# Optimization experiments

Hardware: AMD Instinct MI355X
Metric: run time of the kernel (lower is better)

## Reference

```python
import jax, jax.numpy as jnp
import numpy as np

DIM = 2048
N_HEADS = 32
N_KV_HEADS = 8
HEAD_DIM = 64
REPEATS = N_HEADS // N_KV_HEADS
SLIDING_WINDOW = 1024
EPS = 1e-6
B, T = 2, 2048


def _alibi_slopes(n):
    # n_heads=32 is a power of 2
    r = 2.0 ** (-8.0 / n)
    return jnp.asarray([r ** i for i in range(n)], dtype=jnp.float32)


def _rms_norm(x, w, eps):
    # RMSNorm over the last (flattened heads*head_dim) axis
    var = jnp.mean(x * x, axis=-1, keepdims=True)
    return x * jax.lax.rsqrt(var + eps) * w


def setup_inputs() -> dict:
    key = jax.random.key(0)
    ks = jax.random.split(key, 6)
    s = 0.02
    return {
        "x": jax.random.normal(ks[0], (B, T, DIM), jnp.float32),
        "wq": jax.random.normal(ks[1], (N_HEADS * HEAD_DIM, DIM), jnp.float32) * s,
        "wk": jax.random.normal(ks[2], (N_KV_HEADS * HEAD_DIM, DIM), jnp.float32) * s,
        "wv": jax.random.normal(ks[3], (N_KV_HEADS * HEAD_DIM, DIM), jnp.float32) * s,
        "wo": jax.random.normal(ks[4], (DIM, N_HEADS * HEAD_DIM), jnp.float32) * s,
        "q_norm_w": jnp.ones((N_HEADS * HEAD_DIM,), jnp.float32),
        "k_norm_w": jnp.ones((N_KV_HEADS * HEAD_DIM,), jnp.float32),
    }


def reference(x, wq, wk, wv, wo, q_norm_w, k_norm_w):
    bsz, seqlen, _ = x.shape
    xq = _rms_norm(x @ wq.T, q_norm_w, EPS)
    xk = _rms_norm(x @ wk.T, k_norm_w, EPS)
    xv = x @ wv.T
    xq = xq.reshape(bsz, seqlen, N_HEADS, HEAD_DIM).transpose(0, 2, 1, 3)  # b h t d
    xk = xk.reshape(bsz, seqlen, N_KV_HEADS, HEAD_DIM).transpose(0, 2, 1, 3)
    xv = xv.reshape(bsz, seqlen, N_KV_HEADS, HEAD_DIM).transpose(0, 2, 1, 3)
    # GQA: repeat_interleave kv heads
    xk = jnp.repeat(xk, REPEATS, axis=1)
    xv = jnp.repeat(xv, REPEATS, axis=1)

    pos = jnp.arange(seqlen)
    dist = pos[None, :] - pos[:, None]                     # [t,s] = s - t (<=0 on causal side)
    slopes = _alibi_slopes(N_HEADS)
    alibi = slopes[:, None, None] * dist.astype(jnp.float32)  # [h,t,s]
    allowed = (dist <= 0) & (dist >= -SLIDING_WINDOW)      # causal + sliding window
    bias = jnp.where(allowed[None], alibi, -jnp.inf)       # [h,t,s]

    scale = 1.0 / jnp.sqrt(jnp.asarray(HEAD_DIM, jnp.float32))
    scores = jnp.einsum("bhtd,bhsd->bhts", xq, xk) * scale + bias[None]
    attn = jax.nn.softmax(scores, axis=-1)
    out = jnp.einsum("bhts,bhsd->bhtd", attn, xv)          # [b,h,t,d]
    out = out.transpose(0, 2, 1, 3).reshape(bsz, seqlen, N_HEADS * HEAD_DIM)
    return out @ wo.T
```

## Files before the change

kernel.cpp:

```cpp
#include <hip/hip_runtime.h>


typedef _Float16 f16;
typedef __attribute__((ext_vector_type(8))) _Float16 f16x8;
typedef __attribute__((ext_vector_type(4))) _Float16 f16x4;
typedef __attribute__((ext_vector_type(4))) float f32x4;

#define T_ 2048
#define NH 32
#define NKV 8
#define HD 64
#define WINDOW 1024
#define EPS_ 1e-6f
#define LOG2E 1.44269504088896340736f
#define LDQKV 3072

__device__ inline void async16(void* lds, const void* g) {
  __builtin_amdgcn_global_load_lds(
      (const __attribute__((address_space(1))) unsigned int*)g,
      (__attribute__((address_space(3))) unsigned int*)lds, 16, 0, 0);
}

struct CvtArgs {
  const float* src[5];
  f16* dst[5];
  int n4[5];
};
__global__ __launch_bounds__(256) void cvt_multi(CvtArgs a) {
  const int seg = blockIdx.y;
  const float* in = a.src[seg];
  f16* out = a.dst[seg];
  const int n4 = a.n4[seg];
  for (int i = blockIdx.x * blockDim.x + threadIdx.x; i < n4;
       i += gridDim.x * blockDim.x) {
    float4 v = ((const float4*)in)[i];
    f16x4 o;
    o[0] = (f16)v.x; o[1] = (f16)v.y; o[2] = (f16)v.z; o[3] = (f16)v.w;
    ((f16x4*)out)[i] = o;
  }
}

__global__ __launch_bounds__(256) void gemm_nt(const f16* __restrict__ A,
                                               const f16* __restrict__ B,
                                               void* __restrict__ C,
                                               int M, int N, int K, int ldc,
                                               int out_f32) {
  __shared__ f16 As[128 * 32];
  __shared__ f16 Bs[128 * 32];
  const int tid = threadIdx.x;
  const int lane = tid & 63, wave = tid >> 6;
  const int quad = (lane >> 4), l16 = lane & 15;
  const int wm = (wave >> 1) * 64, wn = (wave & 1) * 64;
  const int m0 = blockIdx.y * 128, n0 = blockIdx.x * 128;
  const int srow = tid >> 2, scol = (tid & 3) * 8;
  const f16* gA = A + (size_t)(m0 + srow) * K + scol;
  const f16* gB = B + (size_t)(n0 + srow) * K + scol;
  f16* lA = As + tid * 8;
  f16* lB = Bs + tid * 8;
  const size_t rowK64 = (size_t)64 * K;

  f32x4 acc[4][4] = {};

  for (int k0 = 0; k0 < K; k0 += 32) {
    async16(lA, gA + k0);
    async16(lA + 2048, gA + rowK64 + k0);
    async16(lB, gB + k0);
    async16(lB + 2048, gB + rowK64 + k0);
    __syncthreads();
    f16x8 af[4], bf[4];
#pragma unroll
    for (int i = 0; i < 4; ++i)
      af[i] = *(const f16x8*)(As + (wm + i * 16 + l16) * 32 + quad * 8);
#pragma unroll
    for (int i = 0; i < 4; ++i)
      bf[i] = *(const f16x8*)(Bs + (wn + i * 16 + l16) * 32 + quad * 8);
#pragma unroll
    for (int i = 0; i < 4; ++i)
#pragma unroll
      for (int j = 0; j < 4; ++j)
        acc[i][j] = __builtin_amdgcn_mfma_f32_16x16x32_f16(af[i], bf[j], acc[i][j], 0, 0, 0);
    __syncthreads();
  }
#pragma unroll
  for (int i = 0; i < 4; ++i) {
    const int row0 = m0 + wm + i * 16 + quad * 4;
#pragma unroll
    for (int j = 0; j < 4; ++j) {
      const int col = n0 + wn + j * 16 + l16;
#pragma unroll
      for (int r = 0; r < 4; ++r) {
        const float v = acc[i][j][r];
        if (out_f32) ((float*)C)[(size_t)(row0 + r) * ldc + col] = v;
        else         ((f16*)C)[(size_t)(row0 + r) * ldc + col] = (f16)v;
      }
    }
  }
}

__global__ __launch_bounds__(256) void rmsnorm2(f16* __restrict__ xqkv,
                                                const float* __restrict__ qw,
                                                const float* __restrict__ kw) {
  __shared__ float red[4];
  const int which = blockIdx.y;
  const int N = which ? 512 : 2048;
  const float* w = which ? kw : qw;
  f16* p = xqkv + (size_t)blockIdx.x * LDQKV + (which ? 2048 : 0);
  const int tid = threadIdx.x;
  const int per = N >> 8;
  float ss = 0.f;
#pragma unroll 4
  for (int i = 0; i < per; ++i) {
    const float v = (float)p[tid * per + i];
    ss += v * v;
  }
#pragma unroll
  for (int off = 32; off > 0; off >>= 1) ss += __shfl_down(ss, off);
  if ((tid & 63) == 0) red[tid >> 6] = ss;
  __syncthreads();
  const float scale = rsqrtf((red[0] + red[1] + red[2] + red[3]) / (float)N + EPS_);
#pragma unroll 4
  for (int i = 0; i < per; ++i) {
    const int c = tid * per + i;
    p[c] = (f16)((float)p[c] * scale * w[c]);
  }
}

__global__ __launch_bounds__(256) void vtrans(const f16* __restrict__ xqkv,
                                              f16* __restrict__ Vt) {
  __shared__ f16 L[64][72];
  const int t0 = blockIdx.x * 64;
  const int b = blockIdx.y >> 3, kh = blockIdx.y & 7;
  const int tid = threadIdx.x;
  const int r = tid >> 3, c = (tid & 7) * 8;
#pragma unroll
  for (int rp = 0; rp < 2; ++rp) {
    const int rr = r + rp * 32;
    *(f16x8*)(&L[rr][c]) =
        *(const f16x8*)(xqkv + (size_t)(b * T_ + t0 + rr) * LDQKV + 2560 + kh * 64 + c);
  }
  __syncthreads();
#pragma unroll
  for (int rp = 0; rp < 2; ++rp) {
    const int d = r + rp * 32;
    f16x8 o;
#pragma unroll
    for (int j = 0; j < 8; ++j) o[j] = L[c + j][d];
    *(f16x8*)(Vt + (size_t)((b * 8 + kh) * 64 + d) * T_ + t0 + c) = o;
  }
}

__global__ __launch_bounds__(256) void attn(const f16* __restrict__ Q,
                                            const f16* __restrict__ Kb,
                                            const f16* __restrict__ Vt_g,
                                            f16* __restrict__ O) {
  constexpr int LDW = 72;
  __shared__ f16 Qs[64 * LDW];
  __shared__ f16 Ks[64 * LDW];
  __shared__ f16 Vts[64 * LDW];
  __shared__ float Lx[4][16];

  const int qt = blockIdx.x, h = blockIdx.y, b = blockIdx.z;
  const int kh = h >> 2;
  const int q0 = qt * 64;
  const int tid = threadIdx.x;
  const int lane = tid & 63, wave = tid >> 6;
  const int quad = lane >> 4, l16 = lane & 15;
  const float scale2 = 0.125f * LOG2E;
  const float slope2 = exp2f(-0.25f * (float)h) * LOG2E;
  const float M2 = 10.0f;

  const int sr = tid >> 3, sc = (tid & 7) * 8;

#pragma unroll
  for (int rp = 0; rp < 2; ++rp) {
    const int rr = sr + rp * 32;
    *(f16x8*)(Qs + rr * LDW + sc) =
        *(const f16x8*)(Q + (size_t)(b * T_ + q0 + rr) * LDQKV + h * HD + sc);
  }
  __syncthreads();
  f16x8 qf[2];
#pragma unroll
  for (int kc = 0; kc < 2; ++kc)
    qf[kc] = *(const f16x8*)(Qs + (wave * 16 + l16) * LDW + kc * 32 + quad * 8);
  f16* Ps = Qs + wave * 16 * LDW;

  f32x4 o_acc[4] = {};
  float lsum = 0.f;

  const int kt_lo = (q0 >= WINDOW) ? ((q0 - WINDOW) >> 6) : 0;
  const int my_q = q0 + wave * 16 + l16;
  const size_t vbase = (size_t)((b * 8 + kh) * 64) * T_;

  float snbr[16];
#pragma unroll
  for (int nb = 0; nb < 4; ++nb)
#pragma unroll
    for (int r = 0; r < 4; ++r) snbr[nb * 4 + r] = slope2 * (float)(nb * 16 + r);
  float base = slope2 * (float)(kt_lo * 64 + quad * 4 - my_q) - M2;
  const float bstep = slope2 * 64.0f;

  f16x8 kreg[2], vreg[2];
  auto prefetch = [&](int k0) {
#pragma unroll
    for (int rp = 0; rp < 2; ++rp) {
      const int rr = sr + rp * 32;
      kreg[rp] = *(const f16x8*)(Kb + (size_t)(b * T_ + k0 + rr) * LDQKV + kh * HD + sc);
      vreg[rp] = *(const f16x8*)(Vt_g + vbase + (size_t)rr * T_ + k0 + sc);
    }
  };
  prefetch(kt_lo * 64);

  for (int kt = kt_lo; kt <= qt; ++kt) {
    const int k0 = kt * 64;
#pragma unroll
    for (int rp = 0; rp < 2; ++rp) {
      *(f16x8*)(Ks + (sr + rp * 32) * LDW + sc) = kreg[rp];
      *(f16x8*)(Vts + (sr + rp * 32) * LDW + sc) = vreg[rp];
    }
    __syncthreads();
    if (kt < qt) prefetch(k0 + 64);

    f32x4 s[4];
#pragma unroll
    for (int nb = 0; nb < 4; ++nb) {
      f32x4 a = {0.f, 0.f, 0.f, 0.f};
#pragma unroll
      for (int kc = 0; kc < 2; ++kc) {
        f16x8 kf = *(const f16x8*)(Ks + (nb * 16 + l16) * LDW + kc * 32 + quad * 8);
        a = __builtin_amdgcn_mfma_f32_16x16x32_f16(kf, qf[kc], a, 0, 0, 0);
      }
      s[nb] = a;
    }

    const bool maskt = (kt == qt) || (q0 + 63 - k0 > WINDOW);
#pragma unroll
    for (int nb = 0; nb < 4; ++nb) {
      f16x4 pk;
#pragma unroll
      for (int r = 0; r < 4; ++r) {
        float v = fmaf(s[nb][r], scale2, base + snbr[nb * 4 + r]);
        if (maskt) {
          const int dist = k0 + nb * 16 + quad * 4 + r - my_q;
          if (dist > 0 || dist < -WINDOW) v = -1e30f;
        }
        const float p = __builtin_amdgcn_exp2f(v);
        lsum += p;
        pk[r] = (f16)p;
      }
      *(f16x4*)(Ps + l16 * LDW + nb * 16 + quad * 4) = pk;
    }
    base += bstep;

#pragma unroll
    for (int nb = 0; nb < 4; ++nb) {
#pragma unroll
      for (int kc = 0; kc < 2; ++kc) {
        f16x8 pa = *(const f16x8*)(Ps + l16 * LDW + kc * 32 + quad * 8);
        f16x8 vb = *(const f16x8*)(Vts + (nb * 16 + l16) * LDW + kc * 32 + quad * 8);
        o_acc[nb] = __builtin_amdgcn_mfma_f32_16x16x32_f16(pa, vb, o_acc[nb], 0, 0, 0);
      }
    }
    __syncthreads();
  }

  lsum += __shfl_xor(lsum, 16);
  lsum += __shfl_xor(lsum, 32);
  if (quad == 0) Lx[wave][l16] = lsum;
  float rl[4];
#pragma unroll
  for (int r = 0; r < 4; ++r) rl[r] = 1.0f / Lx[wave][quad * 4 + r];

#pragma unroll
  for (int r = 0; r < 4; ++r) {
    const int q = q0 + wave * 16 + quad * 4 + r;
#pragma unroll
    for (int nb = 0; nb < 4; ++nb)
      O[(size_t)(b * T_ + q) * (NH * HD) + h * HD + nb * 16 + l16] =
          (f16)(o_acc[nb][r] * rl[r]);
  }
}

extern "C" void kernel_launch(void* const* d_in, const int* in_sizes, int n_in,
                              void* d_out, int out_size, void* d_ws, size_t ws_size,
                              hipStream_t stream) {
  const float* x  = (const float*)d_in[0];
  const float* wq = (const float*)d_in[1];
  const float* wk = (const float*)d_in[2];
  const float* wv = (const float*)d_in[3];
  const float* wo = (const float*)d_in[4];
  const float* qw = (const float*)d_in[5];
  const float* kw = (const float*)d_in[6];
  float* out = (float*)d_out;

  char* ws = (char*)d_ws;
  size_t off = 0;
  auto carve = [&](size_t bytes) -> char* {
    char* p = ws + off;
    off += (bytes + 255) & ~(size_t)255;
    return p;
  };
  f16* xh    = (f16*)carve((size_t)4096 * 2048 * 2);
  f16* wqkvh = (f16*)carve((size_t)3072 * 2048 * 2);
  f16* woh   = (f16*)carve((size_t)2048 * 2048 * 2);
  f16* xqkv  = (f16*)carve((size_t)4096 * 3072 * 2);
  f16* Vt = wqkvh + (size_t)2048 * 2048;
  f16* ao = xh;

  CvtArgs ca;
  ca.src[0] = x;  ca.dst[0] = xh;                            ca.n4[0] = (4096 * 2048) / 4;
  ca.src[1] = wq; ca.dst[1] = wqkvh;                         ca.n4[1] = (2048 * 2048) / 4;
  ca.src[2] = wk; ca.dst[2] = wqkvh + (size_t)2048 * 2048;   ca.n4[2] = (512 * 2048) / 4;
  ca.src[3] = wv; ca.dst[3] = wqkvh + (size_t)2560 * 2048;   ca.n4[3] = (512 * 2048) / 4;
  ca.src[4] = wo; ca.dst[4] = woh;                           ca.n4[4] = (2048 * 2048) / 4;
  cvt_multi<<<dim3(1024, 5), 256, 0, stream>>>(ca);

  gemm_nt<<<dim3(24, 32), 256, 0, stream>>>(xh, wqkvh, xqkv, 4096, 3072, 2048, LDQKV, 0);
  rmsnorm2<<<dim3(4096, 2), 256, 0, stream>>>(xqkv, qw, kw);
  vtrans<<<dim3(32, 16), 256, 0, stream>>>(xqkv, Vt);
  attn<<<dim3(32, 32, 2), 256, 0, stream>>>(xqkv, xqkv + 2048, Vt, ao);
  gemm_nt<<<dim3(16, 32), 256, 0, stream>>>(ao, woh, out, 4096, 2048, 2048, 2048, 1);
}
```

Baseline: 328.1 us.

## Share GQA K/V tiles across four heads per block and fuse norm with V transpose

The attention kernel now launches one block per KV head, with each of the four waves handling a different query head over all 64 query rows. Each K/V tile loaded into LDS is therefore reused by four heads instead of being reloaded by four separate blocks. The RMSNorm and V-transpose kernels are merged into one launch to drop a kernel boundary. In exchange, the grid shrinks to 512 blocks and register pressure rises sharply (16 accumulators plus 8 Q fragments per wave), which could lower occupancy and hurt latency hiding.

```diff
diff --git a/kernel.cpp b/kernel.cpp
--- a/kernel.cpp
+++ b/kernel.cpp
@@ -97,15 +97,41 @@
   }
 }
 
-__global__ __launch_bounds__(256) void rmsnorm2(f16* __restrict__ xqkv,
-                                                const float* __restrict__ qw,
-                                                const float* __restrict__ kw) {
+__global__ __launch_bounds__(256) void norm_vtrans(f16* __restrict__ xqkv,
+                                                   const float* __restrict__ qw,
+                                                   const float* __restrict__ kw,
+                                                   f16* __restrict__ Vt) {
+  const int tid = threadIdx.x;
+  if (blockIdx.y == 2) {
+    if (blockIdx.x >= 512) return;
+    __shared__ f16 L[64][72];
+    const int bx = blockIdx.x;
+    const int t0 = (bx & 31) * 64;
+    const int hb = bx >> 5;
+    const int b = hb >> 3, kh = hb & 7;
+    const int r = tid >> 3, c = (tid & 7) * 8;
+#pragma unroll
+    for (int rp = 0; rp < 2; ++rp) {
+      const int rr = r + rp * 32;
+      *(f16x8*)(&L[rr][c]) =
+          *(const f16x8*)(xqkv + (size_t)(b * T_ + t0 + rr) * LDQKV + 2560 + kh * 64 + c);
+    }
+    __syncthreads();
+#pragma unroll
+    for (int rp = 0; rp < 2; ++rp) {
+      const int d = r + rp * 32;
+      f16x8 o;
+#pragma unroll
+      for (int j = 0; j < 8; ++j) o[j] = L[c + j][d];
+      *(f16x8*)(Vt + (size_t)((b * 8 + kh) * 64 + d) * T_ + t0 + c) = o;
+    }
+    return;
+  }
   __shared__ float red[4];
   const int which = blockIdx.y;
   const int N = which ? 512 : 2048;
   const float* w = which ? kw : qw;
   f16* p = xqkv + (size_t)blockIdx.x * LDQKV + (which ? 2048 : 0);
-  const int tid = threadIdx.x;
   const int per = N >> 8;
   float ss = 0.f;
 #pragma unroll 4
@@ -125,80 +151,64 @@
   }
 }
 
-__global__ __launch_bounds__(256) void vtrans(const f16* __restrict__ xqkv,
-                                              f16* __restrict__ Vt) {
-  __shared__ f16 L[64][72];
-  const int t0 = blockIdx.x * 64;
-  const int b = blockIdx.y >> 3, kh = blockIdx.y & 7;
-  const int tid = threadIdx.x;
-  const int r = tid >> 3, c = (tid & 7) * 8;
-#pragma unroll
-  for (int rp = 0; rp < 2; ++rp) {
-    const int rr = r + rp * 32;
-    *(f16x8*)(&L[rr][c]) =
-        *(const f16x8*)(xqkv + (size_t)(b * T_ + t0 + rr) * LDQKV + 2560 + kh * 64 + c);
-  }
-  __syncthreads();
-#pragma unroll
-  for (int rp = 0; rp < 2; ++rp) {
-    const int d = r + rp * 32;
-    f16x8 o;
-#pragma unroll
-    for (int j = 0; j < 8; ++j) o[j] = L[c + j][d];
-    *(f16x8*)(Vt + (size_t)((b * 8 + kh) * 64 + d) * T_ + t0 + c) = o;
-  }
-}
-
 __global__ __launch_bounds__(256) void attn(const f16* __restrict__ Q,
                                             const f16* __restrict__ Kb,
                                             const f16* __restrict__ Vt_g,
                                             f16* __restrict__ O) {
+  constexpr int LDQ = 68;
   constexpr int LDW = 72;
-  __shared__ f16 Qs[64 * LDW];
+  __shared__ f16 QP[4][64 * LDQ];
   __shared__ f16 Ks[64 * LDW];
   __shared__ f16 Vts[64 * LDW];
-  __shared__ float Lx[4][16];
-
-  const int qt = blockIdx.x, h = blockIdx.y, b = blockIdx.z;
-  const int kh = h >> 2;
+  __shared__ float Lx[4][4][16];
+
+  const int qt = blockIdx.x, kh = blockIdx.y, b = blockIdx.z;
   const int q0 = qt * 64;
   const int tid = threadIdx.x;
   const int lane = tid & 63, wave = tid >> 6;
   const int quad = lane >> 4, l16 = lane & 15;
+  const int h = kh * 4 + wave;
   const float scale2 = 0.125f * LOG2E;
   const float slope2 = exp2f(-0.25f * (float)h) * LOG2E;
   const float M2 = 10.0f;
 
+  f16* Qw = &QP[wave][0];
+
+  {
+    const int r = lane >> 3, c = (lane & 7) * 8;
+#pragma unroll
+    for (int i = 0; i < 8; ++i) {
+      const int row = r + i * 8;
+      *(f16x8*)(Qw + row * LDQ + c) =
+          *(const f16x8*)(Q + (size_t)(b * T_ + q0 + row) * LDQKV + h * HD + c);
+    }
+  }
+  f16x8 qf[4][2];
+#pragma unroll
+  for (int qb = 0; qb < 4; ++qb)
+#pragma unroll
+    for (int kc = 0; kc < 2; ++kc)
+      qf[qb][kc] = *(const f16x8*)(Qw + (qb * 16 + l16) * LDQ + kc * 32 + quad * 8);
+  f16* Ps = Qw;
+
+  f32x4 o_acc[4][4] = {};
+  float lsum[4] = {};
+
+  const int kt_lo = (q0 >= WINDOW) ? ((q0 - WINDOW) >> 6) : 0;
+  const size_t vbase = (size_t)((b * 8 + kh) * 64) * T_;
+
+  float base[4];
+#pragma unroll
+  for (int qb = 0; qb < 4; ++qb)
+    base[qb] = slope2 * (float)(kt_lo * 64 + quad * 4 - (q0 + qb * 16 + l16)) - M2;
+  const float bstep = slope2 * 64.0f;
+  float snr[16];
+#pragma unroll
+  for (int nb = 0; nb < 4; ++nb)
+#pragma unroll
+    for (int r = 0; r < 4; ++r) snr[nb * 4 + r] = slope2 * (float)(nb * 16 + r);
+
   const int sr = tid >> 3, sc = (tid & 7) * 8;
-
-#pragma unroll
-  for (int rp = 0; rp < 2; ++rp) {
-    const int rr = sr + rp * 32;
-    *(f16x8*)(Qs + rr * LDW + sc) =
-        *(const f16x8*)(Q + (size_t)(b * T_ + q0 + rr) * LDQKV + h * HD + sc);
-  }
-  __syncthreads();
-  f16x8 qf[2];
-#pragma unroll
-  for (int kc = 0; kc < 2; ++kc)
-    qf[kc] = *(const f16x8*)(Qs + (wave * 16 + l16) * LDW + kc * 32 + quad * 8);
-  f16* Ps = Qs + wave * 16 * LDW;
-
-  f32x4 o_acc[4] = {};
-  float lsum = 0.f;
-
-  const int kt_lo = (q0 >= WINDOW) ? ((q0 - WINDOW) >> 6) : 0;
-  const int my_q = q0 + wave * 16 + l16;
-  const size_t vbase = (size_t)((b * 8 + kh) * 64) * T_;
-
-  float snbr[16];
-#pragma unroll
-  for (int nb = 0; nb < 4; ++nb)
-#pragma unroll
-    for (int r = 0; r < 4; ++r) snbr[nb * 4 + r] = slope2 * (float)(nb * 16 + r);
-  float base = slope2 * (float)(kt_lo * 64 + quad * 4 - my_q) - M2;
-  const float bstep = slope2 * 64.0f;
-
   f16x8 kreg[2], vreg[2];
   auto prefetch = [&](int k0) {
 #pragma unroll
@@ -220,63 +230,73 @@
     __syncthreads();
     if (kt < qt) prefetch(k0 + 64);
 
-    f32x4 s[4];
+    const bool maskt = (kt == qt) || (q0 + 63 - k0 > WINDOW);
 #pragma unroll
     for (int nb = 0; nb < 4; ++nb) {
-      f32x4 a = {0.f, 0.f, 0.f, 0.f};
-#pragma unroll
-      for (int kc = 0; kc < 2; ++kc) {
-        f16x8 kf = *(const f16x8*)(Ks + (nb * 16 + l16) * LDW + kc * 32 + quad * 8);
-        a = __builtin_amdgcn_mfma_f32_16x16x32_f16(kf, qf[kc], a, 0, 0, 0);
+      f16x8 kf0 = *(const f16x8*)(Ks + (nb * 16 + l16) * LDW + quad * 8);
+      f16x8 kf1 = *(const f16x8*)(Ks + (nb * 16 + l16) * LDW + 32 + quad * 8);
+#pragma unroll
+      for (int qb = 0; qb < 4; ++qb) {
+        f32x4 s = {0.f, 0.f, 0.f, 0.f};
+        s = __builtin_amdgcn_mfma_f32_16x16x32_f16(kf0, qf[qb][0], s, 0, 0, 0);
+        s = __builtin_amdgcn_mfma_f32_16x16x32_f16(kf1, qf[qb][1], s, 0, 0, 0);
+        f16x4 pk;
+#pragma unroll
+        for (int r = 0; r < 4; ++r) {
+          float v = fmaf(s[r], scale2, base[qb] + snr[nb * 4 + r]);
+          if (maskt) {
+            const int dist = k0 + nb * 16 + quad * 4 + r - (q0 + qb * 16 + l16);
+            if (dist > 0 || dist < -WINDOW) v = -1e30f;
+          }
+          const float p = __builtin_amdgcn_exp2f(v);
+          lsum[qb] += p;
+          pk[r] = (f16)p;
+        }
+        *(f16x4*)(Ps + (qb * 16 + l16) * LDQ + nb * 16 + quad * 4) = pk;
       }
-      s[nb] = a;
-    }
-
-    const bool maskt = (kt == qt) || (q0 + 63 - k0 > WINDOW);
-#pragma unroll
-    for (int nb = 0; nb < 4; ++nb) {
-      f16x4 pk;
-#pragma unroll
-      for (int r = 0; r < 4; ++r) {
-        float v = fmaf(s[nb][r], scale2, base + snbr[nb * 4 + r]);
-        if (maskt) {
-          const int dist = k0 + nb * 16 + quad * 4 + r - my_q;
-          if (dist > 0 || dist < -WINDOW) v = -1e30f;
-        }
-        const float p = __builtin_amdgcn_exp2f(v);
-        lsum += p;
-        pk[r] = (f16)p;
+    }
+#pragma unroll
+    for (int qb = 0; qb < 4; ++qb) base[qb] += bstep;
+
+    f16x8 vb[4][2];
+#pragma unroll
+    for (int nb = 0; nb < 4; ++nb)
+#pragma unroll
+      for (int kc = 0; kc < 2; ++kc)
+        vb[nb][kc] = *(const f16x8*)(Vts + (nb * 16 + l16) * LDW + kc * 32 + quad * 8);
+#pragma unroll
+    for (int qb = 0; qb < 4; ++qb) {
+      f16x8 pa0 = *(const f16x8*)(Ps + (qb * 16 + l16) * LDQ + quad * 8);
+      f16x8 pa1 = *(const f16x8*)(Ps + (qb * 16 + l16) * LDQ + 32 + quad * 8);
+#pragma unroll
+      for (int nb = 0; nb < 4; ++nb) {
+        o_acc[nb][qb] = __builtin_amdgcn_mfma_f32_16x16x32_f16(pa0, vb[nb][0], o_acc[nb][qb], 0, 0, 0);
+        o_acc[nb][qb] = __builtin_amdgcn_mfma_f32_16x16x32_f16(pa1, vb[nb][1], o_acc[nb][qb], 0, 0, 0);
       }
-      *(f16x4*)(Ps + l16 * LDW + nb * 16 + quad * 4) = pk;
-    }
-    base += bstep;
-
-#pragma unroll
-    for (int nb = 0; nb < 4; ++nb) {
-#pragma unroll
-      for (int kc = 0; kc < 2; ++kc) {
-        f16x8 pa = *(const f16x8*)(Ps + l16 * LDW + kc * 32 + quad * 8);
-        f16x8 vb = *(const f16x8*)(Vts + (nb * 16 + l16) * LDW + kc * 32 + quad * 8);
-        o_acc[nb] = __builtin_amdgcn_mfma_f32_16x16x32_f16(pa, vb, o_acc[nb], 0, 0, 0);
-      }
-    }
-    __syncthreads();
-  }
-
-  lsum += __shfl_xor(lsum, 16);
-  lsum += __shfl_xor(lsum, 32);
-  if (quad == 0) Lx[wave][l16] = lsum;
-  float rl[4];
-#pragma unroll
-  for (int r = 0; r < 4; ++r) rl[r] = 1.0f / Lx[wave][quad * 4 + r];
-
-#pragma unroll
-  for (int r = 0; r < 4; ++r) {
-    const int q = q0 + wave * 16 + quad * 4 + r;
-#pragma unroll
-    for (int nb = 0; nb < 4; ++nb)
-      O[(size_t)(b * T_ + q) * (NH * HD) + h * HD + nb * 16 + l16] =
-          (f16)(o_acc[nb][r] * rl[r]);
+    }
+    __syncthreads();
+  }
+
+#pragma unroll
+  for (int qb = 0; qb < 4; ++qb) {
+    lsum[qb] += __shfl_xor(lsum[qb], 16);
+    lsum[qb] += __shfl_xor(lsum[qb], 32);
+  }
+  if (lane < 16) {
+#pragma unroll
+    for (int qb = 0; qb < 4; ++qb) Lx[wave][qb][l16] = lsum[qb];
+  }
+#pragma unroll
+  for (int qb = 0; qb < 4; ++qb) {
+#pragma unroll
+    for (int r = 0; r < 4; ++r) {
+      const float rl = 1.0f / Lx[wave][qb][quad * 4 + r];
+      const int q = q0 + qb * 16 + quad * 4 + r;
+#pragma unroll
+      for (int nb = 0; nb < 4; ++nb)
+        O[(size_t)(b * T_ + q) * (NH * HD) + h * HD + nb * 16 + l16] =
+            (f16)(o_acc[nb][qb][r] * rl);
+    }
   }
 }
 
@@ -315,8 +335,7 @@
   cvt_multi<<<dim3(1024, 5), 256, 0, stream>>>(ca);
 
   gemm_nt<<<dim3(24, 32), 256, 0, stream>>>(xh, wqkvh, xqkv, 4096, 3072, 2048, LDQKV, 0);
-  rmsnorm2<<<dim3(4096, 2), 256, 0, stream>>>(xqkv, qw, kw);
-  vtrans<<<dim3(32, 16), 256, 0, stream>>>(xqkv, Vt);
-  attn<<<dim3(32, 32, 2), 256, 0, stream>>>(xqkv, xqkv + 2048, Vt, ao);
+  norm_vtrans<<<dim3(4096, 3), 256, 0, stream>>>(xqkv, qw, kw, Vt);
+  attn<<<dim3(32, 8, 2), 256, 0, stream>>>(xqkv, xqkv + 2048, Vt, ao);
   gemm_nt<<<dim3(16, 32), 256, 0, stream>>>(ao, woh, out, 4096, 2048, 2048, 2048, 1);
 }
```

Result: slower. 369.8 us (+12.7%).
